# Kernel tuning notes

Measured on AMD Instinct MI355X. Metric: run time of the kernel, lower is better.

The kernel has to match this reference:

```python
import jax, jax.numpy as jnp
import numpy as np

TOP_K = 2
EPS = 1e-9


def setup_inputs() -> dict:
    key = jax.random.key(0)
    ks = jax.random.split(key, 5)
    B, S, D, H, E, G = 4, 2048, 1024, 1024, 8, 256
    x = jax.random.normal(ks[0], (B, S, D), dtype=jnp.float32)
    # gate MLP (top_k_gating with hidden_size=gating_size)
    Wg1 = jax.random.normal(ks[1], (D, G), dtype=jnp.float32) * (1.0 / np.sqrt(D))
    Wg2 = jax.random.normal(ks[2], (G, E), dtype=jnp.float32) * (1.0 / np.sqrt(G))
    # experts: uniform(-1/D, 1/D) as in init_experts
    W_in = jax.random.uniform(ks[3], (E, D, H), dtype=jnp.float32, minval=-1.0 / D, maxval=1.0 / D)
    W_out = jax.random.uniform(ks[4], (E, H, D), dtype=jnp.float32, minval=-1.0 / D, maxval=1.0 / D)
    return {"x": x, "Wg1": Wg1, "Wg2": Wg2, "W_in": W_in, "W_out": W_out}


def _gate(xf, Wg1, Wg2):
    # gate MLP -> softmax probs over experts
    h = jnp.tanh(xf @ Wg1)                      # [N, G]
    probs = jax.nn.softmax(h @ Wg2, axis=-1)    # [N, E]
    top_v, top_i = jax.lax.top_k(probs, TOP_K)  # [N, k]
    N, E = probs.shape
    # dense gate matrix: zeros except top-k entries (== compute_gating combine weights)
    gates = jnp.zeros((N, E), probs.dtype).at[jnp.arange(N)[:, None], top_i].set(top_v)
    return gates, probs


def _mi_loss(probs):
    # mutual-information aux loss: minimize -(H(mean_p) - mean H(p))
    p_mean = probs.mean(axis=0)
    h_mean = -jnp.sum(p_mean * jnp.log(p_mean + EPS))
    mean_h = -jnp.mean(jnp.sum(probs * jnp.log(probs + EPS), axis=-1))
    return -h_mean + mean_h


def reference(x, Wg1, Wg2, W_in, W_out):
    B, S, D = x.shape
    xf = x.reshape(-1, D)                        # [N, D]
    gates, probs = _gate(xf, Wg1, Wg2)           # [N, E]
    # per-expert FFN: relu(x @ W_in[e]) @ W_out[e], combined with top-k gates.
    h = jnp.einsum('nd,edh->enh', xf, W_in)      # [E, N, H]
    h = jax.nn.relu(h)
    y = jnp.einsum('enh,ehd->end', h, W_out)     # [E, N, D]
    out = jnp.einsum('ne,end->nd', gates, y)     # gate-weighted combine
    loss = _mi_loss(probs)
    return out.reshape(B, S, D), loss
```

## Files before the change

### kernel.cpp

```cpp
#include <hip/hip_runtime.h>


#define N_TOK 8192
#define DIM   1024
#define HID   1024
#define NEXP  8
#define GDIM  256
#define NPAIR (N_TOK * 2)
#define HB_ROWS (NPAIR + 256)
#define MT2   72
#define GAP_P 2e-3f
#define SPLIT_SCALE 2048.0f
#define NPREP1 (4096 + 64 + 1)

typedef __attribute__((ext_vector_type(4))) float    f32x4;
typedef __attribute__((ext_vector_type(8))) _Float16 f16x8;

static __device__ __forceinline__ void async_ld16(const void* g, void* l) {
  __builtin_amdgcn_global_load_lds(
      (const __attribute__((address_space(1))) unsigned int*)g,
      (__attribute__((address_space(3))) unsigned int*)l, 16, 0, 0);
}

__global__ __launch_bounds__(256) void prep1_kernel(const float* __restrict__ x,
                                                    _Float16* __restrict__ xh,
                                                    const float* __restrict__ Wg1,
                                                    _Float16* __restrict__ WhT,
                                                    _Float16* __restrict__ WlT,
                                                    int* __restrict__ hdr) {
  __shared__ float t[64][65];
  int bx = blockIdx.x;
  int tid = threadIdx.x;
  if (bx < 4096) {
    size_t o = ((size_t)bx * 256 + tid) * 8;
    float4 v0 = *(const float4*)(x + o);
    float4 v1 = *(const float4*)(x + o + 4);
    float v[8] = {v0.x, v0.y, v0.z, v0.w, v1.x, v1.y, v1.z, v1.w};
    f16x8 h;
#pragma unroll
    for (int k = 0; k < 8; ++k) h[k] = (_Float16)v[k];
    *(f16x8*)(xh + o) = h;
  } else if (bx < 4096 + 64) {
    int b = bx - 4096;
    int k0 = (b & 15) * 64, g0 = (b >> 4) * 64;
    int col4 = tid & 15, ib = tid >> 4;
#pragma unroll
    for (int q = 0; q < 4; ++q) {
      int i = ib * 4 + q;
      *(float4*)&t[i][col4 * 4] = *(const float4*)&Wg1[(size_t)(k0 + i) * GDIM + g0 + col4 * 4];
    }
    __syncthreads();
#pragma unroll
    for (int q = 0; q < 2; ++q) {
      int c = tid * 2 + q;
      int j = c >> 3, i8 = (c & 7) * 8;
      f16x8 h, l;
#pragma unroll
      for (int k = 0; k < 8; ++k) {
        float v = t[i8 + k][j];
        _Float16 hi = (_Float16)v;
        h[k] = hi;
        l[k] = (_Float16)((v - (float)hi) * SPLIT_SCALE);
      }
      *(f16x8*)&WhT[(size_t)(g0 + j) * DIM + k0 + i8] = h;
      *(f16x8*)&WlT[(size_t)(g0 + j) * DIM + k0 + i8] = l;
    }
  } else {
    hdr[tid * 2 + 0] = 0;
    hdr[tid * 2 + 1] = 0;
  }
}

__global__ __launch_bounds__(256) void gate_cast_kernel(const _Float16* __restrict__ xh,
                                                        const _Float16* __restrict__ WhT,
                                                        const _Float16* __restrict__ WlT,
                                                        const float* __restrict__ Wg2,
                                                        int* __restrict__ top_i,
                                                        float* __restrict__ top_v,
                                                        float* __restrict__ lossacc,
                                                        int* __restrict__ counts,
                                                        int* __restrict__ nflag,
                                                        int* __restrict__ flaglist,
                                                        const float* __restrict__ Win,
                                                        const float* __restrict__ Wout,
                                                        _Float16* __restrict__ WinT,
                                                        _Float16* __restrict__ WoutT) {
  __shared__ __align__(16) char smem[68096];
  int bx = blockIdx.x;
  int tid = threadIdx.x;

  if (bx >= 256) {
    float (*t)[65] = (float(*)[65])smem;
    int b = bx - 256;
    int z = b >> 8, rem = b & 255;
    const float* src = (z < NEXP ? Win : Wout) + (size_t)(z & 7) * DIM * HID;
    _Float16*    dst = (z < NEXP ? WinT : WoutT) + (size_t)(z & 7) * DIM * HID;
    int i0 = (rem & 15) * 64, j0 = (rem >> 4) * 64;
    int col4 = tid & 15, ib = tid >> 4;
#pragma unroll
    for (int q = 0; q < 4; ++q) {
      int i = ib * 4 + q;
      *(float4*)&t[i][col4 * 4] = *(const float4*)&src[(size_t)(i0 + i) * 1024 + j0 + col4 * 4];
    }
    __syncthreads();
#pragma unroll
    for (int q = 0; q < 2; ++q) {
      int c = tid * 2 + q;
      int j = c >> 3, i8 = (c & 7) * 8;
      f16x8 h;
#pragma unroll
      for (int k = 0; k < 8; ++k) h[k] = (_Float16)t[i8 + k][j];
      *(f16x8*)&dst[(size_t)(j0 + j) * 1024 + i0 + i8] = h;
    }
    return;
  }

  _Float16* Ah = (_Float16*)smem;
  _Float16* Bh = (_Float16*)(smem + 2048);
  _Float16* Bl = (_Float16*)(smem + 18432);
  float (*hsm)[260] = (float(*)[260])(smem + 34816);
  __shared__ float psum[8];
  __shared__ float entsum;
  __shared__ int cnts[8];
  int m0 = bx * 32;
  int lane = tid & 63, wave = tid >> 6;
  int wr = (wave >> 1) * 16;
  int wc = (wave & 1) * 128;
  if (tid < 8) { psum[tid] = 0.f; cnts[tid] = 0; }
  if (tid == 0) entsum = 0.f;

  int srcslot = ((lane & 3) ^ ((lane >> 4) & 3)) << 3;
  size_t asrc = (size_t)(m0 + wave * 16 + (lane >> 2)) * DIM + srcslot;
  size_t bsrc[4];
#pragma unroll
  for (int p = 0; p < 4; ++p)
    bsrc[p] = (size_t)(wave * 16 + p * 64 + (lane >> 2)) * DIM + srcslot;
  int rdoff = ((lane >> 4) ^ ((lane >> 2) & 3)) << 3;
  f32x4 acc[8] = {}, accl[8] = {};

  for (int k0 = 0; k0 < DIM; k0 += 32) {
    __syncthreads();
    if (wave < 2) async_ld16(xh + asrc + k0, Ah + wave * 512);
#pragma unroll
    for (int p = 0; p < 4; ++p) {
      async_ld16(WhT + bsrc[p] + k0, Bh + wave * 512 + p * 2048);
      async_ld16(WlT + bsrc[p] + k0, Bl + wave * 512 + p * 2048);
    }
    __syncthreads();
    f16x8 a = *(const f16x8*)&Ah[(wr + (lane & 15)) * 32 + rdoff];
#pragma unroll
    for (int n = 0; n < 8; ++n) {
      f16x8 bh = *(const f16x8*)&Bh[(wc + n * 16 + (lane & 15)) * 32 + rdoff];
      f16x8 bl = *(const f16x8*)&Bl[(wc + n * 16 + (lane & 15)) * 32 + rdoff];
      acc[n]  = __builtin_amdgcn_mfma_f32_16x16x32_f16(a, bh, acc[n], 0, 0, 0);
      accl[n] = __builtin_amdgcn_mfma_f32_16x16x32_f16(a, bl, accl[n], 0, 0, 0);
    }
  }
#pragma unroll
  for (int n = 0; n < 8; ++n) {
#pragma unroll
    for (int i = 0; i < 4; ++i) {
      int row = wr + ((lane >> 4) << 2) + i;
      int col = wc + n * 16 + (lane & 15);
      hsm[row][col] = tanhf(acc[n][i] + accl[n][i] * (1.0f / SPLIT_SCALE));
    }
  }
  __syncthreads();

  int tok = tid >> 3, sl = tid & 7;
  float lg[8] = {0, 0, 0, 0, 0, 0, 0, 0};
#pragma unroll
  for (int j = 0; j < 32; ++j) {
    int g = sl + j * 8;
    float hv = hsm[tok][g];
#pragma unroll
    for (int e = 0; e < 8; ++e) lg[e] = fmaf(hv, Wg2[g * 8 + e], lg[e]);
  }
#pragma unroll
  for (int e = 0; e < 8; ++e) {
    lg[e] += __shfl_xor(lg[e], 4);
    lg[e] += __shfl_xor(lg[e], 2);
    lg[e] += __shfl_xor(lg[e], 1);
  }
  if (sl == 0) {
    int token = m0 + tok;
    float mx = lg[0];
#pragma unroll
    for (int e = 1; e < 8; ++e) mx = fmaxf(mx, lg[e]);
    float p[8], s = 0.f;
#pragma unroll
    for (int e = 0; e < 8; ++e) { p[e] = expf(lg[e] - mx); s += p[e]; }
    float inv = 1.f / s, ent = 0.f;
    int i0 = 0, i1 = 0;
    float v0 = -1.f, v1 = -1.f, v2 = -1.f;
#pragma unroll
    for (int e = 0; e < 8; ++e) {
      p[e] *= inv;
      ent += p[e] * logf(p[e] + 1e-9f);
      if (p[e] > v0)      { v2 = v1; v1 = v0; i1 = i0; v0 = p[e]; i0 = e; }
      else if (p[e] > v1) { v2 = v1; v1 = p[e]; i1 = e; }
      else if (p[e] > v2) { v2 = p[e]; }
    }
    top_i[token * 2 + 0] = i0; top_i[token * 2 + 1] = i1;
    top_v[token * 2 + 0] = v0; top_v[token * 2 + 1] = v1;
    if (v1 - v2 < GAP_P) {
      int ix = atomicAdd(nflag, 1);
      if (ix < 8192) flaglist[ix] = token;
    }
#pragma unroll
    for (int e = 0; e < 8; ++e) atomicAdd(&psum[e], p[e]);
    atomicAdd(&entsum, ent);
    atomicAdd(&cnts[i0], 1);
    atomicAdd(&cnts[i1], 1);
  }
  __syncthreads();
  if (tid < 8) { atomicAdd(&lossacc[tid], psum[tid]); atomicAdd(&counts[tid], cnts[tid]); }
  if (tid == 8) atomicAdd(&lossacc[8], entsum);
}

__global__ __launch_bounds__(256) void regate_kernel(const float* __restrict__ x,
                                                     const float* __restrict__ Wg1,
                                                     const float* __restrict__ Wg2,
                                                     const int* __restrict__ nflag,
                                                     const int* __restrict__ flaglist,
                                                     int* __restrict__ top_i,
                                                     float* __restrict__ top_v,
                                                     int* __restrict__ counts) {
  __shared__ float xs[DIM];
  __shared__ float wsum[4][8];
  int tid = threadIdx.x;
  int nf = *nflag; if (nf > 8192) nf = 8192;
  for (int it = blockIdx.x; it < nf; it += gridDim.x) {
    int token = flaglist[it];
    const float* xr = x + (size_t)token * DIM;
    *(float4*)&xs[tid * 4] = *(const float4*)&xr[tid * 4];
    __syncthreads();
    float s0 = 0.f, s1 = 0.f, s2 = 0.f, s3 = 0.f;
    float s4 = 0.f, s5 = 0.f, s6 = 0.f, s7 = 0.f;
    for (int k = 0; k < DIM; k += 8) {
      s0 = fmaf(xs[k + 0], Wg1[(size_t)(k + 0) * GDIM + tid], s0);
      s1 = fmaf(xs[k + 1], Wg1[(size_t)(k + 1) * GDIM + tid], s1);
      s2 = fmaf(xs[k + 2], Wg1[(size_t)(k + 2) * GDIM + tid], s2);
      s3 = fmaf(xs[k + 3], Wg1[(size_t)(k + 3) * GDIM + tid], s3);
      s4 = fmaf(xs[k + 4], Wg1[(size_t)(k + 4) * GDIM + tid], s4);
      s5 = fmaf(xs[k + 5], Wg1[(size_t)(k + 5) * GDIM + tid], s5);
      s6 = fmaf(xs[k + 6], Wg1[(size_t)(k + 6) * GDIM + tid], s6);
      s7 = fmaf(xs[k + 7], Wg1[(size_t)(k + 7) * GDIM + tid], s7);
    }
    float hgv = tanhf(((s0 + s1) + (s2 + s3)) + ((s4 + s5) + (s6 + s7)));
    float lg[8];
#pragma unroll
    for (int e = 0; e < 8; ++e) lg[e] = hgv * Wg2[tid * 8 + e];
#pragma unroll
    for (int e = 0; e < 8; ++e) {
      lg[e] += __shfl_xor(lg[e], 32);
      lg[e] += __shfl_xor(lg[e], 16);
      lg[e] += __shfl_xor(lg[e], 8);
      lg[e] += __shfl_xor(lg[e], 4);
      lg[e] += __shfl_xor(lg[e], 2);
      lg[e] += __shfl_xor(lg[e], 1);
    }
    int wv = tid >> 6;
    if ((tid & 63) == 0) {
#pragma unroll
      for (int e = 0; e < 8; ++e) wsum[wv][e] = lg[e];
    }
    __syncthreads();
    if (tid == 0) {
      float l[8];
#pragma unroll
      for (int e = 0; e < 8; ++e)
        l[e] = (wsum[0][e] + wsum[1][e]) + (wsum[2][e] + wsum[3][e]);
      float mx = l[0];
#pragma unroll
      for (int e = 1; e < 8; ++e) mx = fmaxf(mx, l[e]);
      float p[8], s = 0.f;
#pragma unroll
      for (int e = 0; e < 8; ++e) { p[e] = expf(l[e] - mx); s += p[e]; }
      float inv = 1.f / s;
      int i0 = 0, i1 = 0;
      float v0 = -1.f, v1 = -1.f;
#pragma unroll
      for (int e = 0; e < 8; ++e) {
        p[e] *= inv;
        if (p[e] > v0)      { v1 = v0; i1 = i0; v0 = p[e]; i0 = e; }
        else if (p[e] > v1) { v1 = p[e]; i1 = e; }
      }
      int oi0 = top_i[token * 2 + 0], oi1 = top_i[token * 2 + 1];
      if (oi0 != i0 || oi1 != i1) {
        atomicSub(&counts[oi0], 1); atomicSub(&counts[oi1], 1);
        atomicAdd(&counts[i0], 1);  atomicAdd(&counts[i1], 1);
      }
      top_i[token * 2 + 0] = i0; top_i[token * 2 + 1] = i1;
      top_v[token * 2 + 0] = v0; top_v[token * 2 + 1] = v1;
    }
    __syncthreads();
  }
}

__global__ __launch_bounds__(256) void fill_kernel(const int* __restrict__ top_i,
                                                   const float* __restrict__ top_v,
                                                   const int* __restrict__ counts,
                                                   int* __restrict__ cursors,
                                                   int* __restrict__ ptok,
                                                   float* __restrict__ pgate,
                                                   int* __restrict__ rowof) {
  __shared__ int lcnt[8];
  __shared__ int lbase[8];
  __shared__ int soff[8];
  int tid = threadIdx.x;
  int n = blockIdx.x * 256 + tid;
  if (tid == 0) {
    int a = 0;
#pragma unroll
    for (int e = 0; e < 8; ++e) { soff[e] = a; a += counts[e]; }
  }
  if (tid < 8) lcnt[tid] = 0;
  __syncthreads();
  int e0 = top_i[n * 2 + 0], e1 = top_i[n * 2 + 1];
  int p0 = atomicAdd(&lcnt[e0], 1);
  int p1 = atomicAdd(&lcnt[e1], 1);
  __syncthreads();
  if (tid < 8) lbase[tid] = atomicAdd(&cursors[tid], lcnt[tid]);
  __syncthreads();
  int r0 = soff[e0] + lbase[e0] + p0;
  int r1 = soff[e1] + lbase[e1] + p1;
  ptok[r0] = n;  pgate[r0] = top_v[n * 2 + 0];  rowof[n * 2 + 0] = r0;
  ptok[r1] = n;  pgate[r1] = top_v[n * 2 + 1];  rowof[n * 2 + 1] = r1;
}

#define GEMM_PIPE(STAGE_EXPR)                                                        \
  STAGE_EXPR(0, 0);                                                                  \
  STAGE_EXPR(32, 1);                                                                 \
  asm volatile("s_waitcnt vmcnt(3)" ::: "memory");                                   \
  __builtin_amdgcn_s_barrier();                                                      \
  int cbuf = 0;                                                                      \
  for (int t = 0; t < 32; ++t) {                                                     \
    f16x8 a[4], b[4];                                                                \
    _Pragma("unroll")                                                                \
    for (int m = 0; m < 4; ++m)                                                      \
      a[m] = *(const f16x8*)&Als[cbuf][(wr + m * 16 + (lane & 15)) * 32 + rdoff];    \
    _Pragma("unroll")                                                                \
    for (int n = 0; n < 4; ++n)                                                      \
      b[n] = *(const f16x8*)&Bls[cbuf][(wc + n * 16 + (lane & 15)) * 32 + rdoff];    \
    asm volatile("s_waitcnt lgkmcnt(0)" ::: "memory");                               \
    __builtin_amdgcn_sched_barrier(0);                                               \
    __builtin_amdgcn_s_barrier();                                                    \
    bool st = (t + 2 < 32);                                                          \
    if (st) { STAGE_EXPR((t + 2) * 32, cbuf); }                                      \
    __builtin_amdgcn_s_setprio(1);                                                   \
    _Pragma("unroll")                                                                \
    for (int m = 0; m < 4; ++m)                                                      \
      _Pragma("unroll")                                                              \
      for (int n = 0; n < 4; ++n)                                                    \
        acc[m][n] = __builtin_amdgcn_mfma_f32_16x16x32_f16(a[m], b[n], acc[m][n], 0, 0, 0); \
    __builtin_amdgcn_s_setprio(0);                                                   \
    if (st) asm volatile("s_waitcnt vmcnt(3)" ::: "memory");                         \
    else    asm volatile("s_waitcnt vmcnt(0)" ::: "memory");                         \
    __builtin_amdgcn_sched_barrier(0);                                               \
    __builtin_amdgcn_s_barrier();                                                    \
    cbuf ^= 1;                                                                       \
  }

__global__ __launch_bounds__(512) void gemm1_kernel(const _Float16* __restrict__ xh,
                                                    const _Float16* __restrict__ WinT,
                                                    _Float16* __restrict__ hb,
                                                    const int* __restrict__ counts,
                                                    const int* __restrict__ ptok) {
  __shared__ __align__(16) _Float16 Als[2][256 * 32];
  __shared__ __align__(16) _Float16 Bls[2][128 * 32];
  int bx = blockIdx.x;
  int loc = (bx & 7) * 9 + (bx >> 3);
  int base = 0, cnt = 0, e;
  for (e = 0; e < NEXP; ++e) {
    cnt = counts[e];
    int mts = (cnt + 255) >> 8;
    if (loc < mts) break;
    loc -= mts; base += cnt;
  }
  if (e == NEXP) return;
  int row0 = base + (loc << 8);
  int rmax = cnt - (loc << 8);
  int n0 = blockIdx.y << 7;
  int tid = threadIdx.x, wave = tid >> 6, lane = tid & 63;
  int wr = (wave >> 1) << 6, wc = (wave & 1) << 6;

  const _Float16* WB = WinT + (size_t)e * DIM * HID;
  int scol = (((lane & 3) ^ (lane >> 4)) << 3);
  size_t asrc[2];
#pragma unroll
  for (int j = 0; j < 2; ++j) {
    int r = wave * 32 + j * 16 + (lane >> 2);
    int tok = ptok[(r < rmax) ? (row0 + r) : base];
    asrc[j] = (size_t)tok * DIM + scol;
  }
  int brow = tid >> 2;
  size_t bsrc = (size_t)(n0 + brow) * DIM + (((tid & 3) ^ ((tid >> 4) & 3)) << 3);
  int aldst = wave * 1024;
  int bldst = wave * 512;
  int rdoff = ((lane >> 4) ^ ((lane >> 2) & 3)) << 3;
  f32x4 acc[4][4] = {};

#define STAGE1(K0, CB)                                          \
  do {                                                          \
    async_ld16(xh + asrc[0] + (K0), &Als[(CB)][aldst]);         \
    async_ld16(xh + asrc[1] + (K0), &Als[(CB)][aldst + 512]);   \
    async_ld16(WB + bsrc + (K0), &Bls[(CB)][bldst]);            \
  } while (0)

  GEMM_PIPE(STAGE1)
#undef STAGE1

#pragma unroll
  for (int m = 0; m < 4; ++m) {
#pragma unroll
    for (int i = 0; i < 4; ++i) {
      int r = wr + m * 16 + ((lane >> 4) << 2) + i;
      if (r < rmax) {
        _Float16* hrow = hb + (size_t)(row0 + r) * HID;
#pragma unroll
        for (int n = 0; n < 4; ++n)
          hrow[n0 + wc + n * 16 + (lane & 15)] = (_Float16)fmaxf(acc[m][n][i], 0.f);
      }
    }
  }
}

__global__ __launch_bounds__(512) void gemm2_kernel(const _Float16* __restrict__ hb,
                                                    const _Float16* __restrict__ WoutT,
                                                    _Float16* __restrict__ yb,
                                                    const int* __restrict__ counts,
                                                    const float* __restrict__ pgate) {
  __shared__ __align__(16) _Float16 Als[2][256 * 32];
  __shared__ __align__(16) _Float16 Bls[2][128 * 32];
  int bx = blockIdx.x;
  int loc = (bx & 7) * 9 + (bx >> 3);
  int base = 0, cnt = 0, e;
  for (e = 0; e < NEXP; ++e) {
    cnt = counts[e];
    int mts = (cnt + 255) >> 8;
    if (loc < mts) break;
    loc -= mts; base += cnt;
  }
  if (e == NEXP) return;
  int row0 = base + (loc << 8);
  int rmax = cnt - (loc << 8);
  int n0 = blockIdx.y << 7;
  int tid = threadIdx.x, wave = tid >> 6, lane = tid & 63;
  int wr = (wave >> 1) << 6, wc = (wave & 1) << 6;

  const _Float16* WB = WoutT + (size_t)e * DIM * HID;
  int scol = (((lane & 3) ^ (lane >> 4)) << 3);
  size_t asrc[2];
#pragma unroll
  for (int j = 0; j < 2; ++j) {
    int r = wave * 32 + j * 16 + (lane >> 2);
    asrc[j] = (size_t)(row0 + r) * HID + scol;
  }
  int brow = tid >> 2;
  size_t bsrc = (size_t)(n0 + brow) * DIM + (((tid & 3) ^ ((tid >> 4) & 3)) << 3);
  int aldst = wave * 1024;
  int bldst = wave * 512;
  int rdoff = ((lane >> 4) ^ ((lane >> 2) & 3)) << 3;
  f32x4 acc[4][4] = {};

#define STAGE2(K0, CB)                                          \
  do {                                                          \
    async_ld16(hb + asrc[0] + (K0), &Als[(CB)][aldst]);         \
    async_ld16(hb + asrc[1] + (K0), &Als[(CB)][aldst + 512]);   \
    async_ld16(WB + bsrc + (K0), &Bls[(CB)][bldst]);            \
  } while (0)

  GEMM_PIPE(STAGE2)
#undef STAGE2

#pragma unroll
  for (int m = 0; m < 4; ++m) {
#pragma unroll
    for (int i = 0; i < 4; ++i) {
      int r = wr + m * 16 + ((lane >> 4) << 2) + i;
      if (r < rmax) {
        int gr = row0 + r;
        float gv = pgate[gr];
        _Float16* yrow = yb + (size_t)gr * DIM;
#pragma unroll
        for (int n = 0; n < 4; ++n)
          yrow[n0 + wc + n * 16 + (lane & 15)] = (_Float16)(gv * acc[m][n][i]);
      }
    }
  }
}

__global__ __launch_bounds__(256) void combine_kernel(const _Float16* __restrict__ yb,
                                                      const int* __restrict__ rowof,
                                                      float* __restrict__ out,
                                                      const float* __restrict__ lossacc,
                                                      float* __restrict__ lossdst) {
  int tid = threadIdx.x;
  int token = blockIdx.x * 2 + (tid >> 7);
  int d0 = (tid & 127) * 8;
  int r0 = rowof[token * 2 + 0];
  int r1 = rowof[token * 2 + 1];
  f16x8 a = *(const f16x8*)&yb[(size_t)r0 * DIM + d0];
  f16x8 b = *(const f16x8*)&yb[(size_t)r1 * DIM + d0];
  float* orow = out + (size_t)token * DIM + d0;
  float4 o0, o1;
  o0.x = (float)a[0] + (float)b[0]; o0.y = (float)a[1] + (float)b[1];
  o0.z = (float)a[2] + (float)b[2]; o0.w = (float)a[3] + (float)b[3];
  o1.x = (float)a[4] + (float)b[4]; o1.y = (float)a[5] + (float)b[5];
  o1.z = (float)a[6] + (float)b[6]; o1.w = (float)a[7] + (float)b[7];
  *(float4*)orow = o0;
  *(float4*)(orow + 4) = o1;
  if (blockIdx.x == 0 && tid == 0) {
    float t1 = 0.f;
#pragma unroll
    for (int e = 0; e < 8; ++e) {
      float pm = lossacc[e] * (1.f / (float)N_TOK);
      t1 += pm * logf(pm + 1e-9f);
    }
    lossdst[0] = t1 - lossacc[8] * (1.f / (float)N_TOK);
  }
}

extern "C" void kernel_launch(void* const* d_in, const int* in_sizes, int n_in,
                              void* d_out, int out_size, void* d_ws, size_t ws_size,
                              hipStream_t stream) {
  const float* x    = (const float*)d_in[0];
  const float* Wg1  = (const float*)d_in[1];
  const float* Wg2  = (const float*)d_in[2];
  const float* Win  = (const float*)d_in[3];
  const float* Wout = (const float*)d_in[4];
  float* out = (float*)d_out;

  char* ws = (char*)d_ws;
  size_t off = 0;
  auto alloc = [&](size_t bytes) -> void* {
    void* p = ws + off;
    off = (off + bytes + 255) & ~(size_t)255;
    return p;
  };
  int*   counts  = (int*)alloc(32);
  int*   cursors = (int*)alloc(32);
  float* lossacc = (float*)alloc(64);
  int*   nflag   = (int*)alloc(32);
  int*   flaglist= (int*)alloc(8192 * 4);
  int*   top_i   = (int*)alloc((size_t)NPAIR * 4);
  float* top_v   = (float*)alloc((size_t)NPAIR * 4);
  int*   ptok    = (int*)alloc((size_t)NPAIR * 4);
  float* pgate   = (float*)alloc((size_t)NPAIR * 4);
  int*   rowof   = (int*)alloc((size_t)NPAIR * 4);
  char*  scratch1 = (char*)alloc((size_t)HB_ROWS * HID * 2);
  _Float16* Wg1hT  = (_Float16*)scratch1;
  _Float16* Wg1lsT = Wg1hT + (size_t)GDIM * DIM;
  _Float16* hb     = (_Float16*)scratch1;
  _Float16* xh    = (_Float16*)alloc((size_t)N_TOK * DIM * 2);
  _Float16* WinT  = (_Float16*)alloc((size_t)NEXP * DIM * HID * 2);
  _Float16* WoutT = (_Float16*)alloc((size_t)NEXP * DIM * HID * 2);
  _Float16* yb = xh;
  (void)ws_size; (void)in_sizes; (void)n_in;

  prep1_kernel<<<NPREP1, 256, 0, stream>>>(x, xh, Wg1, Wg1hT, Wg1lsT, (int*)d_ws);
  gate_cast_kernel<<<256 + 4096, 256, 0, stream>>>(xh, Wg1hT, Wg1lsT, Wg2, top_i, top_v,
                                                   lossacc, counts, nflag, flaglist,
                                                   Win, Wout, WinT, WoutT);
  regate_kernel<<<256, 256, 0, stream>>>(x, Wg1, Wg2, nflag, flaglist, top_i, top_v, counts);
  fill_kernel<<<N_TOK / 256, 256, 0, stream>>>(top_i, top_v, counts, cursors,
                                               ptok, pgate, rowof);
  gemm1_kernel<<<dim3(MT2, HID / 128), 512, 0, stream>>>(xh, WinT, hb, counts, ptok);
  gemm2_kernel<<<dim3(MT2, DIM / 128), 512, 0, stream>>>(hb, WoutT, yb, counts, pgate);
  combine_kernel<<<N_TOK / 2, 256, 0, stream>>>(yb, rowof, out, lossacc,
                                                out + (size_t)N_TOK * DIM);
}
```

Before: 246.1 us.

## Fuse x fp16 cast into gate kernel and read fp32 x directly in gate GEMM

The x-to-fp16 cast moves out of the serial prep1 kernel and becomes extra blocks of gate_cast_kernel, so it runs at the same time as the gate GEMM and the weight transposes. The gate GEMM now loads fp32 x and converts it to fp16 in registers while staging, so it no longer waits for a separate xh buffer. prep1 shrinks to the Wg1 split and header clear. The cost is synchronous global loads in place of async LDS loads in the gate GEMM, and twice the read bytes for its A tile.

```diff
diff --git a/kernel.cpp b/kernel.cpp
--- a/kernel.cpp
+++ b/kernel.cpp
@@ -11,7 +11,6 @@
 #define MT2   72
 #define GAP_P 2e-3f
 #define SPLIT_SCALE 2048.0f
-#define NPREP1 (4096 + 64 + 1)
 
 typedef __attribute__((ext_vector_type(4))) float    f32x4;
 typedef __attribute__((ext_vector_type(8))) _Float16 f16x8;
@@ -22,27 +21,15 @@
       (__attribute__((address_space(3))) unsigned int*)l, 16, 0, 0);
 }
 
-__global__ __launch_bounds__(256) void prep1_kernel(const float* __restrict__ x,
-                                                    _Float16* __restrict__ xh,
-                                                    const float* __restrict__ Wg1,
+__global__ __launch_bounds__(256) void prep1_kernel(const float* __restrict__ Wg1,
                                                     _Float16* __restrict__ WhT,
                                                     _Float16* __restrict__ WlT,
                                                     int* __restrict__ hdr) {
   __shared__ float t[64][65];
   int bx = blockIdx.x;
   int tid = threadIdx.x;
-  if (bx < 4096) {
-    size_t o = ((size_t)bx * 256 + tid) * 8;
-    float4 v0 = *(const float4*)(x + o);
-    float4 v1 = *(const float4*)(x + o + 4);
-    float v[8] = {v0.x, v0.y, v0.z, v0.w, v1.x, v1.y, v1.z, v1.w};
-    f16x8 h;
-#pragma unroll
-    for (int k = 0; k < 8; ++k) h[k] = (_Float16)v[k];
-    *(f16x8*)(xh + o) = h;
-  } else if (bx < 4096 + 64) {
-    int b = bx - 4096;
-    int k0 = (b & 15) * 64, g0 = (b >> 4) * 64;
+  if (bx < 64) {
+    int k0 = (bx & 15) * 64, g0 = (bx >> 4) * 64;
     int col4 = tid & 15, ib = tid >> 4;
 #pragma unroll
     for (int q = 0; q < 4; ++q) {
@@ -71,7 +58,8 @@
   }
 }
 
-__global__ __launch_bounds__(256) void gate_cast_kernel(const _Float16* __restrict__ xh,
+__global__ __launch_bounds__(256) void gate_cast_kernel(const float* __restrict__ x,
+                                                        _Float16* __restrict__ xh,
                                                         const _Float16* __restrict__ WhT,
                                                         const _Float16* __restrict__ WlT,
                                                         const float* __restrict__ Wg2,
@@ -89,6 +77,16 @@
   int bx = blockIdx.x;
   int tid = threadIdx.x;
 
+  if (bx >= 4352) {
+    size_t o = ((size_t)(bx - 4352) * 256 + tid) * 8;
+    float4 v0 = *(const float4*)(x + o);
+    float4 v1 = *(const float4*)(x + o + 4);
+    f16x8 h;
+    h[0] = (_Float16)v0.x; h[1] = (_Float16)v0.y; h[2] = (_Float16)v0.z; h[3] = (_Float16)v0.w;
+    h[4] = (_Float16)v1.x; h[5] = (_Float16)v1.y; h[6] = (_Float16)v1.z; h[7] = (_Float16)v1.w;
+    *(f16x8*)(xh + o) = h;
+    return;
+  }
   if (bx >= 256) {
     float (*t)[65] = (float(*)[65])smem;
     int b = bx - 256;
@@ -129,8 +127,10 @@
   if (tid < 8) { psum[tid] = 0.f; cnts[tid] = 0; }
   if (tid == 0) entsum = 0.f;
 
+  int arow = tid >> 2, aslt = tid & 3;
+  const float* axsrc = x + (size_t)(m0 + arow) * DIM + ((aslt ^ ((arow >> 2) & 3)) << 3);
+  _Float16* adst = Ah + tid * 8;
   int srcslot = ((lane & 3) ^ ((lane >> 4) & 3)) << 3;
-  size_t asrc = (size_t)(m0 + wave * 16 + (lane >> 2)) * DIM + srcslot;
   size_t bsrc[4];
 #pragma unroll
   for (int p = 0; p < 4; ++p)
@@ -140,7 +140,16 @@
 
   for (int k0 = 0; k0 < DIM; k0 += 32) {
     __syncthreads();
-    if (wave < 2) async_ld16(xh + asrc + k0, Ah + wave * 512);
+    if (tid < 128) {
+      float4 v0 = *(const float4*)(axsrc + k0);
+      float4 v1 = *(const float4*)(axsrc + k0 + 4);
+      f16x8 hv;
+      hv[0] = (_Float16)v0.x; hv[1] = (_Float16)v0.y;
+      hv[2] = (_Float16)v0.z; hv[3] = (_Float16)v0.w;
+      hv[4] = (_Float16)v1.x; hv[5] = (_Float16)v1.y;
+      hv[6] = (_Float16)v1.z; hv[7] = (_Float16)v1.w;
+      *(f16x8*)adst = hv;
+    }
 #pragma unroll
     for (int p = 0; p < 4; ++p) {
       async_ld16(WhT + bsrc[p] + k0, Bh + wave * 512 + p * 2048);
@@ -559,10 +568,11 @@
   _Float16* yb = xh;
   (void)ws_size; (void)in_sizes; (void)n_in;
 
-  prep1_kernel<<<NPREP1, 256, 0, stream>>>(x, xh, Wg1, Wg1hT, Wg1lsT, (int*)d_ws);
-  gate_cast_kernel<<<256 + 4096, 256, 0, stream>>>(xh, Wg1hT, Wg1lsT, Wg2, top_i, top_v,
-                                                   lossacc, counts, nflag, flaglist,
-                                                   Win, Wout, WinT, WoutT);
+  prep1_kernel<<<65, 256, 0, stream>>>(Wg1, Wg1hT, Wg1lsT, (int*)d_ws);
+  gate_cast_kernel<<<256 + 4096 + 4096, 256, 0, stream>>>(x, xh, Wg1hT, Wg1lsT, Wg2,
+                                                          top_i, top_v, lossacc, counts,
+                                                          nflag, flaglist,
+                                                          Win, Wout, WinT, WoutT);
   regate_kernel<<<256, 256, 0, stream>>>(x, Wg1, Wg2, nflag, flaglist, top_i, top_v, counts);
   fill_kernel<<<N_TOK / 256, 256, 0, stream>>>(top_i, top_v, counts, cursors,
                                                ptok, pgate, rowof);
```

New measurement: 246.3 us. Within noise of the previous version (+0.1%).
